# Kernel tuning notes

Measured on AMD Instinct MI355X. Metric: run time of the kernel, lower is better.

## Reference

```python
import jax, jax.numpy as jnp
import numpy as np

AH, AW = 8, 8            # aligned_height, aligned_width
SCALE = 0.0625           # spatial_scale = 1/16
IMG = 1024               # image size implied by 64x64 feature map at stride 16


def setup_inputs() -> dict:
    key = jax.random.key(0)
    k1, k2, k3, k4, k5 = jax.random.split(key, 5)
    B, C, H, W = 4, 256, 64, 64
    N = 2000
    features = jax.random.normal(k1, (B, C, H, W), dtype=jnp.float32)
    # ROIs: (batch_idx, x1, y1, x2, y2) in image coordinates
    bidx = jax.random.randint(k2, (N,), 0, B).astype(jnp.float32)
    cx = jax.random.uniform(k3, (N,), minval=0.0, maxval=IMG)
    cy = jax.random.uniform(k4, (N,), minval=0.0, maxval=IMG)
    wh = jax.random.uniform(k5, (N, 2), minval=32.0, maxval=512.0)
    x1 = jnp.clip(cx - wh[:, 0] / 2, 0.0, IMG - 1.0)
    y1 = jnp.clip(cy - wh[:, 1] / 2, 0.0, IMG - 1.0)
    x2 = jnp.clip(cx + wh[:, 0] / 2, x1 + 16.0, float(IMG))
    y2 = jnp.clip(cy + wh[:, 1] / 2, y1 + 16.0, float(IMG))
    rois = jnp.stack([bidx, x1, y1, x2, y2], axis=1).astype(jnp.float32)
    return {"features": features, "rois": rois}


def _roi_align(features, rois):
    # Classic RoIAlign (crop_and_resize style): one bilinear sample per output
    # cell, sample grid spans the ROI with (aligned-1) intervals.
    B, C, H, W = features.shape
    N = rois.shape[0]
    b = rois[:, 0].astype(jnp.int32)
    x1 = rois[:, 1] * SCALE
    y1 = rois[:, 2] * SCALE
    x2 = rois[:, 3] * SCALE
    y2 = rois[:, 4] * SCALE
    bin_h = (y2 - y1) / (AH - 1.0)
    bin_w = (x2 - x1) / (AW - 1.0)
    ys = y1[:, None, None] + bin_h[:, None, None] * jnp.arange(AH, dtype=jnp.float32)[None, :, None]
    xs = x1[:, None, None] + bin_w[:, None, None] * jnp.arange(AW, dtype=jnp.float32)[None, None, :]
    ys = jnp.broadcast_to(ys, (N, AH, AW))
    xs = jnp.broadcast_to(xs, (N, AH, AW))
    valid = (ys >= 0) & (ys < H) & (xs >= 0) & (xs < W)
    y0 = jnp.floor(ys)
    x0 = jnp.floor(xs)
    ly = ys - y0  # bilinear weights
    lx = xs - x0
    iy0 = jnp.clip(y0.astype(jnp.int32), 0, H - 1)
    ix0 = jnp.clip(x0.astype(jnp.int32), 0, W - 1)
    iy1 = jnp.clip(iy0 + 1, 0, H - 1)
    ix1 = jnp.clip(ix0 + 1, 0, W - 1)
    bb = b[:, None, None]

    def g(iy, ix):
        return features[bb, :, iy, ix]  # [N, AH, AW, C]

    ly_ = ly[..., None]
    lx_ = lx[..., None]
    v = ((1 - ly_) * (1 - lx_) * g(iy0, ix0)
         + (1 - ly_) * lx_ * g(iy0, ix1)
         + ly_ * (1 - lx_) * g(iy1, ix0)
         + ly_ * lx_ * g(iy1, ix1))
    v = jnp.where(valid[..., None], v, 0.0)
    return jnp.transpose(v, (0, 3, 1, 2))  # [N, C, AH, AW]


def _max_pool_2x2_s1(x):
    # max_pool2d(kernel_size=2, stride=1): [N,C,h,w] -> [N,C,h-1,w-1]
    return jnp.maximum(
        jnp.maximum(x[:, :, :-1, :-1], x[:, :, :-1, 1:]),
        jnp.maximum(x[:, :, 1:, :-1], x[:, :, 1:, 1:]),
    )


def reference(features, rois):
    x = _roi_align(features, rois)
    return _max_pool_2x2_s1(x)  # [N, C, AH-1, AW-1]
```

## Files before the change

kernel.cpp:

```cpp
#include <hip/hip_runtime.h>
#include <cstdint>

constexpr int CCH = 256;
constexpr int HH  = 64;
constexpr int WW  = 64;
constexpr int OHW = 49;
constexpr float RSCALE = 0.0625f;

#define FMUL __fmul_rn
#define FADD __fadd_rn
#define FSUB __fsub_rn
#define FDIV __fdiv_rn

typedef float v4f __attribute__((ext_vector_type(4)));

__device__ __forceinline__ float4 f4max(float4 a, float4 b) {
  return make_float4(fmaxf(a.x, b.x), fmaxf(a.y, b.y),
                     fmaxf(a.z, b.z), fmaxf(a.w, b.w));
}

__device__ __forceinline__ unsigned short f2bf(float f) {
  union { float f; unsigned u; } a; a.f = f;
  unsigned u = a.u;
  u += 0x7fffu + ((u >> 16) & 1u);
  return (unsigned short)(u >> 16);
}

__device__ __forceinline__ float4 bf4_to_f4(uint2 u) {
  float4 r;
  r.x = __uint_as_float(u.x << 16);
  r.y = __uint_as_float(u.x & 0xffff0000u);
  r.z = __uint_as_float(u.y << 16);
  r.w = __uint_as_float(u.y & 0xffff0000u);
  return r;
}

__global__ __launch_bounds__(256) void ktrans_sched(const float* __restrict__ in,
                                                    unsigned short* __restrict__ out,
                                                    const float* __restrict__ rois,
                                                    int N, int slots, int do_sched,
                                                    int B, int* __restrict__ meta) {
  const int t = threadIdx.x;

  if ((int)blockIdx.z == B) {
    if (blockIdx.x != 0 || blockIdx.y != 0 || !do_sched) return;
    __shared__ int cnt[4], rnk[4], off[4], slack[4], excess[4];
    if (t < 4) { cnt[t] = 0; rnk[t] = 0; }
    __syncthreads();
    for (int i = t; i < N; i += 256) atomicAdd(&cnt[(int)rois[i * 5]], 1);
    __syncthreads();
    if (t == 0) {
      int o = 0, cs = 0, ce = 0;
      for (int p = 0; p < 4; ++p) {
        off[p] = o; o += cnt[p];
        slack[p]  = cs; if (slots - cnt[p] > 0) cs += slots - cnt[p];
        excess[p] = ce; if (cnt[p] - slots > 0) ce += cnt[p] - slots;
        meta[p] = cnt[p]; meta[4 + p] = off[p]; meta[8 + p] = slack[p];
      }
    }
    __syncthreads();
    int* perm = meta + 16;
    for (int i = t; i < N; i += 256) {
      const int b = (int)rois[i * 5];
      perm[off[b] + atomicAdd(&rnk[b], 1)] = i;
    }
    __syncthreads();
    int* extra = meta + 16 + N;
    for (int p = 0; p < 4; ++p) {
      const int ex = cnt[p] - slots;
      for (int e = t; e < ex; e += 256) extra[excess[p] + e] = perm[off[p] + slots + e];
    }
    return;
  }

  __shared__ float tile[64][65];
  const int b  = blockIdx.z;
  const int c0 = blockIdx.y * 64;
  const int s0 = blockIdx.x * 64;
  const float* inb = in + (size_t)b * CCH * (HH * WW);
  unsigned short* outb = out + (size_t)b * (HH * WW) * CCH;

  const int cl = t >> 4, sq = t & 15;
#pragma unroll
  for (int k = 0; k < 4; ++k) {
    const int c = cl + 16 * k;
    const v4f v = __builtin_nontemporal_load(
        (const v4f*)(inb + (size_t)(c0 + c) * (HH * WW) + s0 + 4 * sq));
    tile[c][4 * sq + 0] = v[0];
    tile[c][4 * sq + 1] = v[1];
    tile[c][4 * sq + 2] = v[2];
    tile[c][4 * sq + 3] = v[3];
  }
  __syncthreads();
  const int cq = t & 15, rl = t >> 4;
#pragma unroll
  for (int k = 0; k < 4; ++k) {
    const int r = rl + 16 * k;
    ushort4 w;
    w.x = f2bf(tile[4 * cq + 0][r]);
    w.y = f2bf(tile[4 * cq + 1][r]);
    w.z = f2bf(tile[4 * cq + 2][r]);
    w.w = f2bf(tile[4 * cq + 3][r]);
    *(ushort4*)(outb + (size_t)(s0 + r) * CCH + c0 + 4 * cq) = w;
  }
}

__global__ __launch_bounds__(256, 6) void roi_kernel10(const uint2* __restrict__ feat,
                                                       const float* __restrict__ rois,
                                                       const int* __restrict__ meta,
                                                       int N, int use_perm,
                                                       float* __restrict__ out) {
  __shared__ float4 smem4[OHW * 32];
  float* smem = (float*)smem4;
  const int i = blockIdx.x;
  const int t = threadIdx.x;
  const int g = t & 31;
  const int r = t >> 5;

  int n, half;
  if (use_perm) {
    const int p = (i & 7) >> 1;
    half        = i & 1;
    const int s = i >> 3;
    const int c_ = meta[p];
    const int o_ = meta[4 + p];
    const int sl = meta[8 + p];
    const int* perm  = meta + 16;
    const int* extra = meta + 16 + N;
    n = (s < c_) ? perm[o_ + s] : extra[sl + (s - c_)];
  } else {
    n = i >> 1; half = i & 1;
  }

  const float rb = rois[n * 5 + 0];
  const float x1 = FMUL(rois[n * 5 + 1], RSCALE);
  const float y1 = FMUL(rois[n * 5 + 2], RSCALE);
  const float x2 = FMUL(rois[n * 5 + 3], RSCALE);
  const float y2 = FMUL(rois[n * 5 + 4], RSCALE);
  const int   b  = (int)rb;
  const float bh = FDIV(FSUB(y2, y1), 7.0f);
  const float bw = FDIV(FSUB(x2, x1), 7.0f);

  int   xo0[8], xo1[8];
  float lx[8];
  bool  xv[8];
#pragma unroll
  for (int q = 0; q < 8; ++q) {
    const float xs = FADD(x1, FMUL(bw, (float)q));
    xv[q] = (xs >= 0.0f) && (xs < (float)WW);
    const float xf = floorf(xs);
    lx[q] = FSUB(xs, xf);
    int a = (int)xf;
    a = a < 0 ? 0 : (a > WW - 1 ? WW - 1 : a);
    xo0[q] = a * (CCH / 4);
    xo1[q] = ((a + 1 > WW - 1) ? WW - 1 : a + 1) * (CCH / 4);
  }

  const float ys = FADD(y1, FMUL(bh, (float)r));
  const bool  yv = (ys >= 0.0f) && (ys < (float)HH);
  const float yf = floorf(ys);
  const float ly = FSUB(ys, yf);
  int d = (int)yf;
  d = d < 0 ? 0 : (d > HH - 1 ? HH - 1 : d);
  const int d1 = (d + 1 > HH - 1) ? HH - 1 : d + 1;

  const uint2* fb = feat + (size_t)b * (HH * WW) * (CCH / 4) + (half * 32 + g);
  const uint2* r0 = fb + (size_t)d  * (WW * (CCH / 4));
  const uint2* r1 = fb + (size_t)d1 * (WW * (CCH / 4));
  const float wy1 = ly, wy0 = 1.0f - ly;

  float4 hc[7], vprev;
#pragma unroll
  for (int h = 0; h < 2; ++h) {
    uint2 g00[4], g01[4], g10[4], g11[4];
#pragma unroll
    for (int q = 0; q < 4; ++q) {
      const int s = 4 * h + q;
      g00[q] = r0[xo0[s]];
      g01[q] = r0[xo1[s]];
      g10[q] = r1[xo0[s]];
      g11[q] = r1[xo1[s]];
    }
    float4 v[4];
#pragma unroll
    for (int q = 0; q < 4; ++q) {
      const int s = 4 * h + q;
      const bool ok = yv && xv[s];
      const float wx1 = lx[s], wx0 = 1.0f - wx1;
      const float a00 = wy0 * wx0, a01 = wy0 * wx1;
      const float a10 = wy1 * wx0, a11 = wy1 * wx1;
      const float4 f00 = bf4_to_f4(g00[q]);
      const float4 f01 = bf4_to_f4(g01[q]);
      const float4 f10 = bf4_to_f4(g10[q]);
      const float4 f11 = bf4_to_f4(g11[q]);
      float4 rr;
      rr.x = a00 * f00.x + a01 * f01.x + a10 * f10.x + a11 * f11.x;
      rr.y = a00 * f00.y + a01 * f01.y + a10 * f10.y + a11 * f11.y;
      rr.z = a00 * f00.z + a01 * f01.z + a10 * f10.z + a11 * f11.z;
      rr.w = a00 * f00.w + a01 * f01.w + a10 * f10.w + a11 * f11.w;
      v[q] = ok ? rr : make_float4(0.f, 0.f, 0.f, 0.f);
    }
    if (h == 0) {
      hc[0] = f4max(v[0], v[1]);
      hc[1] = f4max(v[1], v[2]);
      hc[2] = f4max(v[2], v[3]);
      vprev = v[3];
    } else {
      hc[3] = f4max(vprev, v[0]);
      hc[4] = f4max(v[0], v[1]);
      hc[5] = f4max(v[1], v[2]);
      hc[6] = f4max(v[2], v[3]);
    }
  }

  if (r >= 1) {
#pragma unroll
    for (int m = 0; m < 7; ++m)
      smem4[((r - 1) * 7 + m) * 32 + g] = hc[m];
  }
  __syncthreads();

  if (r <= 6) {
#pragma unroll
    for (int m = 0; m < 7; ++m)
      hc[m] = f4max(hc[m], smem4[(r * 7 + m) * 32 + g]);
#pragma unroll
    for (int m = 0; m < 7; ++m) {
      const int s  = r * 7 + m;
      const int gp = g ^ ((s >> 2) & 7);
      smem4[s * 32 + gp] = hc[m];
    }
  }
  __syncthreads();

  float4* o4 = (float4*)(out + (size_t)n * (CCH * OHW) + half * (CCH / 2) * OHW);
#pragma unroll
  for (int m = 0; m < 7; ++m) {
    const int idx = m * 256 + t;
    if (idx < (CCH / 2) * OHW / 4) {
      const int f0 = idx * 4;
      float4 wv;
      float* wp = (float*)&wv;
#pragma unroll
      for (int k = 0; k < 4; ++k) {
        const int e = f0 + k;
        const int c = e / 49;
        const int s = e - c * 49;
        wp[k] = smem[s * 128 + 4 * ((c >> 2) ^ ((s >> 2) & 7)) + (c & 3)];
      }
      o4[idx] = wv;
    }
  }
}

__global__ __launch_bounds__(256) void roi_kernel_fb(const float* __restrict__ feat,
                                                     const float* __restrict__ rois,
                                                     float* __restrict__ out) {
  __shared__ float sout[CCH * OHW];
  const int n = blockIdx.x;
  const int c = threadIdx.x;

  const float rb = rois[n * 5 + 0];
  const float x1 = FMUL(rois[n * 5 + 1], RSCALE);
  const float y1 = FMUL(rois[n * 5 + 2], RSCALE);
  const float x2 = FMUL(rois[n * 5 + 3], RSCALE);
  const float y2 = FMUL(rois[n * 5 + 4], RSCALE);
  const int b = (int)rb;
  const float bh = FDIV(FSUB(y2, y1), 7.0f);
  const float bw = FDIV(FSUB(x2, x1), 7.0f);

  int ix0[8], ix1[8], iy0[8], iy1[8];
  float lx[8], ly[8];
  bool xv[8], yv[8];
#pragma unroll
  for (int i = 0; i < 8; ++i) {
    const float xs = FADD(x1, FMUL(bw, (float)i));
    const float ys = FADD(y1, FMUL(bh, (float)i));
    xv[i] = (xs >= 0.0f) && (xs < (float)WW);
    yv[i] = (ys >= 0.0f) && (ys < (float)HH);
    const float xf = floorf(xs);
    const float yf = floorf(ys);
    lx[i] = FSUB(xs, xf);
    ly[i] = FSUB(ys, yf);
    int a = (int)xf;
    a = a < 0 ? 0 : (a > WW - 1 ? WW - 1 : a);
    ix0[i] = a;
    ix1[i] = (a + 1 > WW - 1) ? WW - 1 : a + 1;
    int d = (int)yf;
    d = d < 0 ? 0 : (d > HH - 1 ? HH - 1 : d);
    iy0[i] = d;
    iy1[i] = (d + 1 > HH - 1) ? HH - 1 : d + 1;
  }

  const float* fbp = feat + ((size_t)b * CCH + c) * (size_t)(HH * WW);
  float hp[7];
#pragma unroll
  for (int j = 0; j < 8; ++j) {
    float v[8];
    const float wy1 = ly[j], wy0 = 1.0f - ly[j];
#pragma unroll
    for (int i = 0; i < 8; ++i) {
      if (yv[j] && xv[i]) {
        const float f00 = fbp[iy0[j] * WW + ix0[i]];
        const float f01 = fbp[iy0[j] * WW + ix1[i]];
        const float f10 = fbp[iy1[j] * WW + ix0[i]];
        const float f11 = fbp[iy1[j] * WW + ix1[i]];
        const float wx1 = lx[i], wx0 = 1.0f - wx1;
        v[i] = wy0 * (wx0 * f00 + wx1 * f01) + wy1 * (wx0 * f10 + wx1 * f11);
      } else {
        v[i] = 0.0f;
      }
    }
    float hc[7];
#pragma unroll
    for (int i = 0; i < 7; ++i) hc[i] = fmaxf(v[i], v[i + 1]);
    if (j > 0) {
#pragma unroll
      for (int i = 0; i < 7; ++i)
        sout[c * OHW + (j - 1) * 7 + i] = fmaxf(hp[i], hc[i]);
    }
#pragma unroll
    for (int i = 0; i < 7; ++i) hp[i] = hc[i];
  }
  __syncthreads();
  const float4* s4 = (const float4*)sout;
  float4* o4 = (float4*)(out + (size_t)n * (CCH * OHW));
  for (int q = c; q < (CCH * OHW) / 4; q += 256) o4[q] = s4[q];
}

extern "C" void kernel_launch(void* const* d_in, const int* in_sizes, int n_in,
                              void* d_out, int out_size, void* d_ws, size_t ws_size,
                              hipStream_t stream) {
  (void)n_in; (void)out_size;
  const float* feat = (const float*)d_in[0];
  const float* rois = (const float*)d_in[1];
  float* out = (float*)d_out;
  const int N = in_sizes[1] / 5;
  const int B = in_sizes[0] / (CCH * HH * WW);
  const int M = 2 * N;
  const size_t featbf_bytes = (size_t)in_sizes[0] * sizeof(unsigned short);
  const size_t meta_bytes   = (size_t)(16 + 2 * N) * sizeof(int);

  if (ws_size >= featbf_bytes + meta_bytes) {
    unsigned short* featbf = (unsigned short*)d_ws;
    int* meta = (int*)((char*)d_ws + featbf_bytes);
    const int use_perm = (B == 4 && (M & 7) == 0) ? 1 : 0;

    ktrans_sched<<<dim3((HH * WW) / 64, CCH / 64, B + 1), dim3(256), 0, stream>>>(
        feat, featbf, rois, N, M >> 3, use_perm, B, meta);
    roi_kernel10<<<dim3(M), dim3(256), 0, stream>>>(
        (const uint2*)featbf, rois, meta, N, use_perm, out);
  } else {
    roi_kernel_fb<<<dim3(N), dim3(256), 0, stream>>>(feat, rois, out);
  }
}
```

Baseline: 133.6 us.

## Switch feature copy and bilinear math to fp16 packed ops, simplify LDS output staging

The transposed feature copy is now stored as fp16 instead of bf16. The bilinear interpolation and max-pooling in the ROI kernel run in packed half-precision vector arithmetic instead of unpacking to fp32. The final vertical max writes half values into a channel-major LDS buffer, so the output loop does a contiguous 8-byte LDS read and a nontemporal float4 store instead of per-element div/mod gather with XOR swizzle. This cuts ALU and address-math work and LDS footprint per element. In exchange it gives fp16 precision on accumulation and may cause LDS bank conflicts on the scattered half-word writes.

```diff
diff --git a/kernel.cpp b/kernel.cpp
--- a/kernel.cpp
+++ b/kernel.cpp
@@ -12,27 +12,23 @@
 #define FSUB __fsub_rn
 #define FDIV __fdiv_rn
 
-typedef float v4f __attribute__((ext_vector_type(4)));
-
-__device__ __forceinline__ float4 f4max(float4 a, float4 b) {
-  return make_float4(fmaxf(a.x, b.x), fmaxf(a.y, b.y),
-                     fmaxf(a.z, b.z), fmaxf(a.w, b.w));
-}
-
-__device__ __forceinline__ unsigned short f2bf(float f) {
-  union { float f; unsigned u; } a; a.f = f;
-  unsigned u = a.u;
-  u += 0x7fffu + ((u >> 16) & 1u);
-  return (unsigned short)(u >> 16);
-}
-
-__device__ __forceinline__ float4 bf4_to_f4(uint2 u) {
-  float4 r;
-  r.x = __uint_as_float(u.x << 16);
-  r.y = __uint_as_float(u.x & 0xffff0000u);
-  r.z = __uint_as_float(u.y << 16);
-  r.w = __uint_as_float(u.y & 0xffff0000u);
-  return r;
+typedef float     v4f __attribute__((ext_vector_type(4)));
+typedef _Float16  h2  __attribute__((ext_vector_type(2)));
+typedef _Float16  h4  __attribute__((ext_vector_type(4)));
+
+__device__ __forceinline__ h2 pkrtz(float a, float b) {
+  auto t = __builtin_amdgcn_cvt_pkrtz(a, b);
+  union { decltype(t) s; h2 d; } c; c.s = t; return c.d;
+}
+__device__ __forceinline__ h4 bcast4(float a) {
+  h2 t = pkrtz(a, a);
+  return __builtin_shufflevector(t, t, 0, 1, 0, 1);
+}
+__device__ __forceinline__ h4 u2h(uint2 u) {
+  union { uint2 u; h4 h; } c; c.u = u; return c.h;
+}
+__device__ __forceinline__ h4 h4max(h4 a, h4 b) {
+  return __builtin_elementwise_max(a, b);
 }
 
 __global__ __launch_bounds__(256) void ktrans_sched(const float* __restrict__ in,
@@ -96,22 +92,23 @@
 #pragma unroll
   for (int k = 0; k < 4; ++k) {
     const int r = rl + 16 * k;
-    ushort4 w;
-    w.x = f2bf(tile[4 * cq + 0][r]);
-    w.y = f2bf(tile[4 * cq + 1][r]);
-    w.z = f2bf(tile[4 * cq + 2][r]);
-    w.w = f2bf(tile[4 * cq + 3][r]);
-    *(ushort4*)(outb + (size_t)(s0 + r) * CCH + c0 + 4 * cq) = w;
-  }
-}
-
-__global__ __launch_bounds__(256, 6) void roi_kernel10(const uint2* __restrict__ feat,
+    union { h2 h; unsigned u; } p0, p1;
+    p0.h.x = (_Float16)tile[4 * cq + 0][r];
+    p0.h.y = (_Float16)tile[4 * cq + 1][r];
+    p1.h.x = (_Float16)tile[4 * cq + 2][r];
+    p1.h.y = (_Float16)tile[4 * cq + 3][r];
+    uint2 w; w.x = p0.u; w.y = p1.u;
+    *(uint2*)(outb + (size_t)(s0 + r) * CCH + c0 + 4 * cq) = w;
+  }
+}
+
+__global__ __launch_bounds__(256, 6) void roi_kernel11(const uint2* __restrict__ feat,
                                                        const float* __restrict__ rois,
                                                        const int* __restrict__ meta,
                                                        int N, int use_perm,
                                                        float* __restrict__ out) {
-  __shared__ float4 smem4[OHW * 32];
-  float* smem = (float*)smem4;
+  __shared__ __attribute__((aligned(16))) h4       ldsA[OHW * 32];
+  __shared__ __attribute__((aligned(16))) _Float16 ldsC[(CCH / 2) * OHW];
   const int i = blockIdx.x;
   const int t = threadIdx.x;
   const int g = t & 31;
@@ -169,7 +166,7 @@
   const uint2* r1 = fb + (size_t)d1 * (WW * (CCH / 4));
   const float wy1 = ly, wy0 = 1.0f - ly;
 
-  float4 hc[7], vprev;
+  h4 hc[7], vprev;
 #pragma unroll
   for (int h = 0; h < 2; ++h) {
     uint2 g00[4], g01[4], g10[4], g11[4];
@@ -181,74 +178,68 @@
       g10[q] = r1[xo0[s]];
       g11[q] = r1[xo1[s]];
     }
-    float4 v[4];
+    h4 v[4];
 #pragma unroll
     for (int q = 0; q < 4; ++q) {
       const int s = 4 * h + q;
       const bool ok = yv && xv[s];
       const float wx1 = lx[s], wx0 = 1.0f - wx1;
-      const float a00 = wy0 * wx0, a01 = wy0 * wx1;
-      const float a10 = wy1 * wx0, a11 = wy1 * wx1;
-      const float4 f00 = bf4_to_f4(g00[q]);
-      const float4 f01 = bf4_to_f4(g01[q]);
-      const float4 f10 = bf4_to_f4(g10[q]);
-      const float4 f11 = bf4_to_f4(g11[q]);
-      float4 rr;
-      rr.x = a00 * f00.x + a01 * f01.x + a10 * f10.x + a11 * f11.x;
-      rr.y = a00 * f00.y + a01 * f01.y + a10 * f10.y + a11 * f11.y;
-      rr.z = a00 * f00.z + a01 * f01.z + a10 * f10.z + a11 * f11.z;
-      rr.w = a00 * f00.w + a01 * f01.w + a10 * f10.w + a11 * f11.w;
-      v[q] = ok ? rr : make_float4(0.f, 0.f, 0.f, 0.f);
+      const h4 w00 = bcast4(wy0 * wx0);
+      const h4 w01 = bcast4(wy0 * wx1);
+      const h4 w10 = bcast4(wy1 * wx0);
+      const h4 w11 = bcast4(wy1 * wx1);
+      h4 rr = w00 * u2h(g00[q]) + w01 * u2h(g01[q])
+            + w10 * u2h(g10[q]) + w11 * u2h(g11[q]);
+      v[q] = ok ? rr : h4{};
     }
     if (h == 0) {
-      hc[0] = f4max(v[0], v[1]);
-      hc[1] = f4max(v[1], v[2]);
-      hc[2] = f4max(v[2], v[3]);
+      hc[0] = h4max(v[0], v[1]);
+      hc[1] = h4max(v[1], v[2]);
+      hc[2] = h4max(v[2], v[3]);
       vprev = v[3];
     } else {
-      hc[3] = f4max(vprev, v[0]);
-      hc[4] = f4max(v[0], v[1]);
-      hc[5] = f4max(v[1], v[2]);
-      hc[6] = f4max(v[2], v[3]);
+      hc[3] = h4max(vprev, v[0]);
+      hc[4] = h4max(v[0], v[1]);
+      hc[5] = h4max(v[1], v[2]);
+      hc[6] = h4max(v[2], v[3]);
     }
   }
 
   if (r >= 1) {
 #pragma unroll
     for (int m = 0; m < 7; ++m)
-      smem4[((r - 1) * 7 + m) * 32 + g] = hc[m];
+      ldsA[((r - 1) * 7 + m) * 32 + g] = hc[m];
   }
   __syncthreads();
 
   if (r <= 6) {
-#pragma unroll
-    for (int m = 0; m < 7; ++m)
-      hc[m] = f4max(hc[m], smem4[(r * 7 + m) * 32 + g]);
+    _Float16* cb = ldsC + (4 * g) * OHW + r * 7;
 #pragma unroll
     for (int m = 0; m < 7; ++m) {
-      const int s  = r * 7 + m;
-      const int gp = g ^ ((s >> 2) & 7);
-      smem4[s * 32 + gp] = hc[m];
+      const h4 x = h4max(hc[m], ldsA[(r * 7 + m) * 32 + g]);
+      cb[0 * OHW + m] = x[0];
+      cb[1 * OHW + m] = x[1];
+      cb[2 * OHW + m] = x[2];
+      cb[3 * OHW + m] = x[3];
     }
   }
   __syncthreads();
 
-  float4* o4 = (float4*)(out + (size_t)n * (CCH * OHW) + half * (CCH / 2) * OHW);
+  const uint2* cs = (const uint2*)ldsC;
+  v4f* o4 = (v4f*)(out + (size_t)n * (CCH * OHW) + half * (CCH / 2) * OHW);
 #pragma unroll
   for (int m = 0; m < 7; ++m) {
     const int idx = m * 256 + t;
     if (idx < (CCH / 2) * OHW / 4) {
-      const int f0 = idx * 4;
-      float4 wv;
-      float* wp = (float*)&wv;
-#pragma unroll
-      for (int k = 0; k < 4; ++k) {
-        const int e = f0 + k;
-        const int c = e / 49;
-        const int s = e - c * 49;
-        wp[k] = smem[s * 128 + 4 * ((c >> 2) ^ ((s >> 2) & 7)) + (c & 3)];
-      }
-      o4[idx] = wv;
+      const uint2 qv = cs[idx];
+      union { unsigned u; h2 h; } c0, c1;
+      c0.u = qv.x; c1.u = qv.y;
+      v4f wv;
+      wv.x = (float)c0.h.x;
+      wv.y = (float)c0.h.y;
+      wv.z = (float)c1.h.x;
+      wv.w = (float)c1.h.y;
+      __builtin_nontemporal_store(wv, o4 + idx);
     }
   }
 }
@@ -348,7 +339,7 @@
 
     ktrans_sched<<<dim3((HH * WW) / 64, CCH / 64, B + 1), dim3(256), 0, stream>>>(
         feat, featbf, rois, N, M >> 3, use_perm, B, meta);
-    roi_kernel10<<<dim3(M), dim3(256), 0, stream>>>(
+    roi_kernel11<<<dim3(M), dim3(256), 0, stream>>>(
         (const uint2*)featbf, rois, meta, N, use_perm, out);
   } else {
     roi_kernel_fb<<<dim3(N), dim3(256), 0, stream>>>(feat, rois, out);
```

Result: faster. 130.5 us, median of 2 (-2.3%).
